# Kernel tuning notes

Measured on AMD Instinct MI355X. Metric: run time of the kernel, lower is better.

The kernel has to match this reference:

```python
import jax, jax.numpy as jnp
import numpy as np

B, NB, S, K, M, C = 2, 6000, 3, 8, 6, 256
INIT = 0.02


def setup_inputs() -> dict:
    key = jax.random.key(0)
    ks = jax.random.split(key, 24)
    d = {}
    d["pts_query_feats"] = jax.random.normal(ks[0], (B, NB, C), jnp.float32)
    d["pts_query_pe"] = jax.random.normal(ks[1], (B, NB, C), jnp.float32)
    d["knn_feat_seq"] = jax.random.normal(ks[2], (S, B, NB, K, C), jnp.float32)
    d["knn_pe_seq"] = jax.random.normal(ks[3], (S, B, NB, K, C), jnp.float32)
    d["sampled_feat"] = jax.random.normal(ks[4], (B, NB, M, C), jnp.float32)
    d["mask"] = jax.random.bernoulli(ks[5], 0.7, (B, NB, M))  # True = valid image sample
    # per-seq temporal attention params (S cloned single-head MHA modules)
    d["Wq_t"] = INIT * jax.random.normal(ks[6], (S, C, C), jnp.float32)
    d["Wk_t"] = INIT * jax.random.normal(ks[7], (S, C, C), jnp.float32)
    d["Wv_t"] = INIT * jax.random.normal(ks[8], (S, C, C), jnp.float32)
    d["Wo_t"] = INIT * jax.random.normal(ks[9], (S, C, C), jnp.float32)
    d["bq_t"] = jnp.zeros((S, C), jnp.float32)
    d["bk_t"] = jnp.zeros((S, C), jnp.float32)
    d["bv_t"] = jnp.zeros((S, C), jnp.float32)
    d["bo_t"] = jnp.zeros((S, C), jnp.float32)
    # cross-sensor single-head MHA params
    d["Wq_c"] = INIT * jax.random.normal(ks[10], (C, C), jnp.float32)
    d["Wk_c"] = INIT * jax.random.normal(ks[11], (C, C), jnp.float32)
    d["Wv_c"] = INIT * jax.random.normal(ks[12], (C, C), jnp.float32)
    d["Wo_c"] = INIT * jax.random.normal(ks[13], (C, C), jnp.float32)
    d["bq_c"] = jnp.zeros((C,), jnp.float32)
    d["bk_c"] = jnp.zeros((C,), jnp.float32)
    d["bv_c"] = jnp.zeros((C,), jnp.float32)
    d["bo_c"] = jnp.zeros((C,), jnp.float32)
    return d


def reference(pts_query_feats, pts_query_pe, knn_feat_seq, knn_pe_seq,
              sampled_feat, mask,
              Wq_t, Wk_t, Wv_t, Wo_t, bq_t, bk_t, bv_t, bo_t,
              Wq_c, Wk_c, Wv_c, Wo_c, bq_c, bk_c, bv_c, bo_c):
    scale = 1.0 / np.sqrt(C).astype(np.float32)

    # with_pos_embed
    q_base = pts_query_feats + pts_query_pe           # [B,NB,C]
    kv = knn_feat_seq + knn_pe_seq                    # [S,B,NB,K,C]

    # temporal attention: per voxel, 1 query token attends over K knn keys;
    # S distinct (cloned) single-head MHA modules, outputs summed over seq.
    q = jnp.einsum('bnc,scd->sbnd', q_base, Wq_t) + bq_t[:, None, None, :]
    k = jnp.einsum('sbnkc,scd->sbnkd', kv, Wk_t) + bk_t[:, None, None, None, :]
    v = jnp.einsum('sbnkc,scd->sbnkd', kv, Wv_t) + bv_t[:, None, None, None, :]
    scores = jnp.einsum('sbnd,sbnkd->sbnk', q, k) * scale
    attn = jax.nn.softmax(scores, axis=-1)
    ctx = jnp.einsum('sbnk,sbnkd->sbnd', attn, v)
    out_s = jnp.einsum('sbnd,sde->sbne', ctx, Wo_t) + bo_t[:, None, None, :]
    out = out_s.sum(axis=0)                           # [B,NB,C]

    # cross-sensor attention over M image samples; attn_mask = ~mask (True blocks)
    valid = mask.any(axis=-1)                         # [B,NB]
    qc = out @ Wq_c + bq_c                            # [B,NB,C]
    kc = sampled_feat @ Wk_c + bk_c                   # [B,NB,M,C]
    vc = sampled_feat @ Wv_c + bv_c
    sc = jnp.einsum('bnc,bnmc->bnm', qc, kc) * scale
    sc = jnp.where(mask, sc, -1e9)
    a = jax.nn.softmax(sc, axis=-1)
    cctx = jnp.einsum('bnm,bnmc->bnc', a, vc)
    outc = cctx @ Wo_c + bo_c                         # [B,NB,C]

    # original drops invalid voxels; we keep static shape and zero them
    return jnp.where(valid[..., None], outc, 0.0)
```

## Files before the change

### kernel.cpp

```cpp
#include <hip/hip_runtime.h>
#include <math.h>

#define CC 256
#define KK 8
#define MM 6
#define SS 3
#define NVOX 12000
#define VB 16
#define NBLK (NVOX / VB)

typedef __attribute__((ext_vector_type(8))) short bf16x8;
typedef __attribute__((ext_vector_type(4))) float f32x4;
typedef __attribute__((ext_vector_type(4))) float fvec4;

#define OFF_WQKF3  0u
#define OFF_WVOF   262144u
#define OFF_BQK    1048576u
#define OFF_BVO    1052672u
#define OFF_BBIG   1056768u
#define OFF_QK3PK  1057792u
#define OFF_WBIGPK 1451008u
#define OFF_WVOCPK 1844224u
#define WS_NEED    1975296u

__device__ __forceinline__ float wred(float p) {
  #pragma unroll
  for (int off = 32; off; off >>= 1) p += __shfl_xor(p, off, 64);
  return p;
}
__device__ __forceinline__ uint f2bf(float x) {
  const uint u = __float_as_uint(x);
  return (u + 0x7fffu + ((u >> 16) & 1u)) >> 16;
}
__device__ __forceinline__ uint bfpack(float a, float b) {
  return (f2bf(b) << 16) | f2bf(a);
}
__device__ __forceinline__ float bflo(uint w) { return __uint_as_float(w << 16); }
__device__ __forceinline__ float bfhi(uint w) { return __uint_as_float(w & 0xffff0000u); }

__device__ __forceinline__ f32x4 mfma16(bf16x8 a, bf16x8 b, f32x4 c) {
  return __builtin_amdgcn_mfma_f32_16x16x32_bf16(a, b, c, 0, 0, 0);
}

__global__ __launch_bounds__(256) void prep_fold_all(
    const float* __restrict__ Wq_t, const float* __restrict__ Wq_c,
    const float* __restrict__ Wk_t, const float* __restrict__ Wk_c,
    const float* __restrict__ Wv_t, const float* __restrict__ Wv_c,
    const float* __restrict__ Wo_t, const float* __restrict__ Wo_c,
    const float* __restrict__ bq_t, const float* __restrict__ bq_c,
    const float* __restrict__ bv_t, const float* __restrict__ bv_c,
    const float* __restrict__ bo_t, const float* __restrict__ bo_c,
    float* __restrict__ Wqkf3, float* __restrict__ Wvof,
    float* __restrict__ bqk, float* __restrict__ bvo,
    uint4* __restrict__ qk3pk, uint4* __restrict__ wvocpk) {
  const int b = blockIdx.x, t = threadIdx.x;
  if (b < 256) {
    const int u = b >> 5, c0 = (b & 31) * 8;
    __shared__ float xl[8][256];
    const float* X;
    if (u < 4) X = (u < 3) ? (Wq_t + u * 65536) : Wq_c;
    else { const int v = u - 4; X = (v < 3) ? (Wv_t + v * 65536) : Wv_c; }
    #pragma unroll
    for (int i = 0; i < 8; ++i) xl[i][t] = X[(c0 + i) * 256 + t];
    __syncthreads();
    float acc[8] = {0.f, 0.f, 0.f, 0.f, 0.f, 0.f, 0.f, 0.f};
    if (u < 4) {
      const float* Wk = (u < 3) ? (Wk_t + u * 65536) : Wk_c;
      const float4* wr = (const float4*)(Wk + t * 256);
      #pragma unroll 4
      for (int d4 = 0; d4 < 64; ++d4) {
        const float4 wv = wr[d4];
        #pragma unroll
        for (int j = 0; j < 8; ++j) {
          acc[j] += xl[j][d4 * 4] * wv.x + xl[j][d4 * 4 + 1] * wv.y +
                    xl[j][d4 * 4 + 2] * wv.z + xl[j][d4 * 4 + 3] * wv.w;
        }
      }
    } else {
      const int v = u - 4;
      const float* Wo = (v < 3) ? (Wo_t + v * 65536) : Wo_c;
      #pragma unroll 4
      for (int d = 0; d < 256; ++d) {
        const float w = Wo[d * 256 + t];
        #pragma unroll
        for (int j = 0; j < 8; ++j) acc[j] += xl[j][d] * w;
      }
    }
    const int lane = (((c0 >> 3) & 3) << 4) | (t & 15);
    if (u < 3) {
      uint4 o;
      o.x = bfpack(acc[0], acc[1]); o.y = bfpack(acc[2], acc[3]);
      o.z = bfpack(acc[4], acc[5]); o.w = bfpack(acc[6], acc[7]);
      qk3pk[((u * 16 + (t >> 4)) * 8 + (c0 >> 5)) * 64 + lane] = o;
    } else if (u == 3) {
      #pragma unroll
      for (int j = 0; j < 8; ++j) Wqkf3[(c0 + j) * 256 + t] = acc[j];
    } else if (u < 7) {
      const int v = u - 4;
      #pragma unroll
      for (int j = 0; j < 8; ++j) Wvof[(v * 256 + c0 + j) * 256 + t] = acc[j];
    } else {
      uint4 o;
      o.x = bfpack(acc[0], acc[1]); o.y = bfpack(acc[2], acc[3]);
      o.z = bfpack(acc[4], acc[5]); o.w = bfpack(acc[6], acc[7]);
      wvocpk[((t >> 4) * 8 + (c0 >> 5)) * 64 + lane] = o;
    }
  } else {
    const int u = b - 256;
    __shared__ float bql[256], bvl[256];
    const float* bq = (u < 3) ? (bq_t + u * 256) : bq_c;
    const float* bv = (u < 3) ? (bv_t + u * 256) : bv_c;
    const float* bo = (u < 3) ? (bo_t + u * 256) : bo_c;
    bql[t] = bq[t]; bvl[t] = bv[t];
    __syncthreads();
    const float* Wk = (u < 3) ? (Wk_t + u * 65536) : Wk_c;
    const float* Wo = (u < 3) ? (Wo_t + u * 65536) : Wo_c;
    const float4* wr = (const float4*)(Wk + t * 256);
    float a1 = 0.f, a2 = 0.f;
    #pragma unroll 4
    for (int d4 = 0; d4 < 64; ++d4) {
      const float4 wv = wr[d4];
      a1 += bql[d4 * 4] * wv.x + bql[d4 * 4 + 1] * wv.y +
            bql[d4 * 4 + 2] * wv.z + bql[d4 * 4 + 3] * wv.w;
    }
    #pragma unroll 4
    for (int d = 0; d < 256; ++d) a2 += bvl[d] * Wo[d * 256 + t];
    bqk[u * 256 + t] = a1;
    bvo[u * 256 + t] = a2 + bo[t];
  }
}

__global__ __launch_bounds__(256) void prep_wbig2(
    const float* __restrict__ Wvof, const float* __restrict__ Wqkf3,
    const float* __restrict__ bqk, const float* __restrict__ bvo,
    uint4* __restrict__ wbigpk, float* __restrict__ bbig) {
  const int b = blockIdx.x, t = threadIdx.x;
  if (b < 96) {
    const int c0 = b * 8;
    __shared__ float xl[8][256];
    #pragma unroll
    for (int i = 0; i < 8; ++i) xl[i][t] = Wvof[(c0 + i) * 256 + t];
    __syncthreads();
    float acc[8] = {0.f, 0.f, 0.f, 0.f, 0.f, 0.f, 0.f, 0.f};
    #pragma unroll 4
    for (int d = 0; d < 256; ++d) {
      const float w = Wqkf3[d * 256 + t];
      #pragma unroll
      for (int j = 0; j < 8; ++j) acc[j] += xl[j][d] * w;
    }
    uint4 o;
    o.x = bfpack(acc[0], acc[1]); o.y = bfpack(acc[2], acc[3]);
    o.z = bfpack(acc[4], acc[5]); o.w = bfpack(acc[6], acc[7]);
    const int lane = (((c0 >> 3) & 3) << 4) | (t & 15);
    wbigpk[((t >> 4) * 24 + (c0 >> 5)) * 64 + lane] = o;
  } else {
    __shared__ float bvs[256];
    bvs[t] = bvo[t] + bvo[256 + t] + bvo[512 + t];
    __syncthreads();
    float acc = bqk[3 * 256 + t];
    #pragma unroll 4
    for (int d = 0; d < 256; ++d) acc += bvs[d] * Wqkf3[d * 256 + t];
    bbig[t] = acc;
  }
}

__global__ __launch_bounds__(512, 4) void stftr_mega(
    const float* __restrict__ ptsf, const float* __restrict__ ptspe,
    const float* __restrict__ knnf, const float* __restrict__ knnpe,
    const float* __restrict__ sfeat, const int* __restrict__ maskp,
    const bf16x8* __restrict__ qk3pk, const bf16x8* __restrict__ wbigpk,
    const bf16x8* __restrict__ wvocpk,
    const float* __restrict__ bqk, const float* __restrict__ bbig,
    const float* __restrict__ bvoc,
    float* __restrict__ out) {
  __shared__ char shA[25088];
  __shared__ char shB[24832];
  __shared__ int vlds[VB];
  const int t = threadIdx.x, lane = t & 63, w = t >> 6;
  const int g0 = blockIdx.x * VB;

  {
    uint* qb_u = (uint*)shB;
    const float4* a4 = (const float4*)(ptsf + (size_t)g0 * CC);
    const float4* b4 = (const float4*)(ptspe + (size_t)g0 * CC);
    #pragma unroll
    for (int it = 0; it < 2; ++it) {
      const int idx = it * 512 + t;
      const int row = idx >> 6, c4 = idx & 63;
      const float4 va = a4[idx], vb = b4[idx];
      qb_u[row * 132 + c4 * 2]     = bfpack(va.x + vb.x, va.y + vb.y);
      qb_u[row * 132 + c4 * 2 + 1] = bfpack(va.z + vb.z, va.w + vb.w);
    }
  }
  __syncthreads();
  {
    f32x4 acc[6];
    #pragma unroll
    for (int nb = 0; nb < 6; ++nb) acc[nb] = (f32x4){0.f, 0.f, 0.f, 0.f};
    const char* qbase = shB + (lane & 15) * 528 + (lane >> 4) * 16;
    #pragma unroll
    for (int kb = 0; kb < 8; ++kb) {
      const bf16x8 a = *(const bf16x8*)(qbase + kb * 64);
      #pragma unroll
      for (int nb = 0; nb < 6; ++nb) {
        const bf16x8 bb = qk3pk[((w * 6 + nb) * 8 + kb) * 64 + lane];
        acc[nb] = mfma16(a, bb, acc[nb]);
      }
    }
    ushort* us = (ushort*)shA;
    #pragma unroll
    for (int nb = 0; nb < 6; ++nb) {
      const int n = (w * 6 + nb) * 16 + (lane & 15);
      const float bias = bqk[n];
      #pragma unroll
      for (int r = 0; r < 4; ++r) {
        const int row = (lane >> 4) * 4 + r;
        us[row * 776 + n] = (ushort)f2bf(acc[nb][r] + bias);
      }
    }
  }
  __syncthreads();
  {
    const uint* Au = (const uint*)shA;
    uint* Bu = (uint*)shB;
    const fvec4* kfp = (const fvec4*)knnf;
    const fvec4* kpp = (const fvec4*)knnpe;
    #pragma unroll
    for (int q = 0; q < 6; ++q) {
      const int tid = w * 6 + q;
      const int s = tid >> 4, j = tid & 15;
      const size_t rb = ((size_t)(s * NVOX + g0 + j)) * 512 + lane;
      fvec4 sm[KK];
      #pragma unroll
      for (int r = 0; r < KK; ++r) {
        const fvec4 kf = __builtin_nontemporal_load(&kfp[rb + r * 64]);
        const fvec4 kp = __builtin_nontemporal_load(&kpp[rb + r * 64]);
        sm[r] = kf + kp;
      }
      const uint ua = Au[j * 388 + s * 128 + lane * 2];
      const uint ub = Au[j * 388 + s * 128 + lane * 2 + 1];
      const float u0 = bflo(ua), u1 = bfhi(ua), u2 = bflo(ub), u3 = bfhi(ub);
      float sc[KK];
      #pragma unroll
      for (int r = 0; r < KK; ++r) {
        float p = sm[r].x * u0 + sm[r].y * u1 + sm[r].z * u2 + sm[r].w * u3;
        sc[r] = wred(p);
      }
      float mx = sc[0];
      #pragma unroll
      for (int r = 1; r < KK; ++r) mx = fmaxf(mx, sc[r]);
      float e[KK], sum = 0.f;
      #pragma unroll
      for (int r = 0; r < KK; ++r) { e[r] = __expf((sc[r] - mx) * 0.0625f); sum += e[r]; }
      const float inv = 1.f / sum;
      fvec4 acc = (fvec4){0.f, 0.f, 0.f, 0.f};
      #pragma unroll
      for (int r = 0; r < KK; ++r) acc += (e[r] * inv) * sm[r];
      Bu[j * 388 + s * 128 + lane * 2]     = bfpack(acc.x, acc.y);
      Bu[j * 388 + s * 128 + lane * 2 + 1] = bfpack(acc.z, acc.w);
    }
  }
  __syncthreads();
  {
    f32x4 acc[2];
    acc[0] = (f32x4){0.f, 0.f, 0.f, 0.f};
    acc[1] = (f32x4){0.f, 0.f, 0.f, 0.f};
    const char* abase = shB + (lane & 15) * 1552 + (lane >> 4) * 16;
    #pragma unroll 4
    for (int kb = 0; kb < 24; ++kb) {
      const bf16x8 a = *(const bf16x8*)(abase + kb * 64);
      #pragma unroll
      for (int nb = 0; nb < 2; ++nb) {
        const bf16x8 bb = wbigpk[((w * 2 + nb) * 24 + kb) * 64 + lane];
        acc[nb] = mfma16(a, bb, acc[nb]);
      }
    }
    ushort* ust = (ushort*)shA;
    #pragma unroll
    for (int nb = 0; nb < 2; ++nb) {
      const int n = (w * 2 + nb) * 16 + (lane & 15);
      const float bias = bbig[n];
      #pragma unroll
      for (int r = 0; r < 4; ++r) {
        const int row = (lane >> 4) * 4 + r;
        ust[row * 264 + n] = (ushort)f2bf(acc[nb][r] + bias);
      }
    }
  }
  __syncthreads();
  {
    const uint* Au = (const uint*)shA;
    uint* Bu = (uint*)shB;
    const float4* sfp = (const float4*)sfeat;
    #pragma unroll
    for (int jj = 0; jj < 2; ++jj) {
      const int j = w * 2 + jj;
      const int g = g0 + j;
      const uint ua = Au[j * 132 + lane * 2];
      const uint ub = Au[j * 132 + lane * 2 + 1];
      const float u0 = bflo(ua), u1 = bfhi(ua), u2 = bflo(ub), u3 = bfhi(ub);
      const size_t sb = (size_t)g * (MM * 64) + lane;
      float4 sf[MM]; float scm[MM]; int anyv = 0;
      #pragma unroll
      for (int m = 0; m < MM; ++m) {
        sf[m] = sfp[sb + m * 64];
        const int mk = maskp[(size_t)g * MM + m];
        anyv |= mk;
        float p = sf[m].x * u0 + sf[m].y * u1 + sf[m].z * u2 + sf[m].w * u3;
        p = wred(p);
        scm[m] = mk ? p * 0.0625f : -1e9f;
      }
      float mx = scm[0];
      #pragma unroll
      for (int m = 1; m < MM; ++m) mx = fmaxf(mx, scm[m]);
      float e[MM], sum = 0.f;
      #pragma unroll
      for (int m = 0; m < MM; ++m) { e[m] = __expf(scm[m] - mx); sum += e[m]; }
      const float inv = 1.f / sum;
      float4 ag = make_float4(0.f, 0.f, 0.f, 0.f);
      #pragma unroll
      for (int m = 0; m < MM; ++m) {
        const float a = e[m] * inv;
        ag.x += a * sf[m].x; ag.y += a * sf[m].y;
        ag.z += a * sf[m].z; ag.w += a * sf[m].w;
      }
      Bu[j * 132 + lane * 2]     = bfpack(ag.x, ag.y);
      Bu[j * 132 + lane * 2 + 1] = bfpack(ag.z, ag.w);
      if (lane == 0) vlds[j] = anyv;
    }
  }
  __syncthreads();
  {
    f32x4 acc[2];
    acc[0] = (f32x4){0.f, 0.f, 0.f, 0.f};
    acc[1] = (f32x4){0.f, 0.f, 0.f, 0.f};
    const char* cbase = shB + (lane & 15) * 528 + (lane >> 4) * 16;
    #pragma unroll
    for (int kb = 0; kb < 8; ++kb) {
      const bf16x8 a = *(const bf16x8*)(cbase + kb * 64);
      #pragma unroll
      for (int nb = 0; nb < 2; ++nb) {
        const bf16x8 bb = wvocpk[((w * 2 + nb) * 8 + kb) * 64 + lane];
        acc[nb] = mfma16(a, bb, acc[nb]);
      }
    }
    float* ost = (float*)(shA + 8448);
    #pragma unroll
    for (int nb = 0; nb < 2; ++nb) {
      const int n = (w * 2 + nb) * 16 + (lane & 15);
      const float bias = bvoc[n];
      #pragma unroll
      for (int r = 0; r < 4; ++r) {
        const int row = (lane >> 4) * 4 + r;
        ost[row * 260 + n] = acc[nb][r] + bias;
      }
    }
  }
  __syncthreads();
  {
    const float* ost = (const float*)(shA + 8448);
    #pragma unroll
    for (int it = 0; it < 8; ++it) {
      const int idx = it * 512 + t;
      const int row = idx >> 8, d = idx & 255;
      out[((size_t)(g0 + row)) * 256 + d] = vlds[row] ? ost[row * 260 + d] : 0.f;
    }
  }
}

extern "C" void kernel_launch(void* const* d_in, const int* in_sizes, int n_in,
                              void* d_out, int out_size, void* d_ws, size_t ws_size,
                              hipStream_t stream) {
  const float* ptsf  = (const float*)d_in[0];
  const float* ptspe = (const float*)d_in[1];
  const float* knnf  = (const float*)d_in[2];
  const float* knnpe = (const float*)d_in[3];
  const float* sfeat = (const float*)d_in[4];
  const int*   maskp = (const int*)d_in[5];
  const float* Wq_t = (const float*)d_in[6];
  const float* Wk_t = (const float*)d_in[7];
  const float* Wv_t = (const float*)d_in[8];
  const float* Wo_t = (const float*)d_in[9];
  const float* bq_t = (const float*)d_in[10];
  const float* bv_t = (const float*)d_in[12];
  const float* bo_t = (const float*)d_in[13];
  const float* Wq_c = (const float*)d_in[14];
  const float* Wk_c = (const float*)d_in[15];
  const float* Wv_c = (const float*)d_in[16];
  const float* Wo_c = (const float*)d_in[17];
  const float* bq_c = (const float*)d_in[18];
  const float* bv_c = (const float*)d_in[20];
  const float* bo_c = (const float*)d_in[21];

  if (ws_size < WS_NEED) return;
  char* ws = (char*)d_ws;
  float* Wqkf3  = (float*)(ws + OFF_WQKF3);
  float* Wvof   = (float*)(ws + OFF_WVOF);
  float* bqk    = (float*)(ws + OFF_BQK);
  float* bvo    = (float*)(ws + OFF_BVO);
  float* bbig   = (float*)(ws + OFF_BBIG);
  uint4* qk3pk  = (uint4*)(ws + OFF_QK3PK);
  uint4* wbigpk = (uint4*)(ws + OFF_WBIGPK);
  uint4* wvocpk = (uint4*)(ws + OFF_WVOCPK);

  prep_fold_all<<<260, 256, 0, stream>>>(
      Wq_t, Wq_c, Wk_t, Wk_c, Wv_t, Wv_c, Wo_t, Wo_c,
      bq_t, bq_c, bv_t, bv_c, bo_t, bo_c,
      Wqkf3, Wvof, bqk, bvo, qk3pk, wvocpk);
  prep_wbig2<<<97, 256, 0, stream>>>(Wvof, Wqkf3, bqk, bvo, wbigpk, bbig);

  stftr_mega<<<NBLK, 512, 0, stream>>>(
      ptsf, ptspe, knnf, knnpe, sfeat, maskp,
      (const bf16x8*)qk3pk, (const bf16x8*)wbigpk, (const bf16x8*)wvocpk,
      bqk, bbig, bvo + 3 * 256, (float*)d_out);
}
```

Measured before the change: 171.2 us.

## Merge weight-fold prep kernels into one and tune main kernel memory access

Merges the two weight-folding prep kernels into a single launch. Each block now chains the Wv·Wo·Wq_c·Wk_c products itself, which removes the intermediate fp32 workspace and the dependency between two launches. The main kernel raises its occupancy hint from 4 to 6 waves per SIMD and stages the mask in LDS instead of reading it per lane. It also uses nontemporal loads and stores for streamed inputs and output, and drops an unroll on the KNN loop. Tradeoffs: the prep blocks do serial work, and the higher occupancy target may cause register spills.

Measured after the change: 170.2 us. About the same (-0.6%).

```diff
diff --git a/kernel.cpp b/kernel.cpp
--- a/kernel.cpp
+++ b/kernel.cpp
@@ -13,15 +13,13 @@
 typedef __attribute__((ext_vector_type(4))) float f32x4;
 typedef __attribute__((ext_vector_type(4))) float fvec4;
 
-#define OFF_WQKF3  0u
-#define OFF_WVOF   262144u
-#define OFF_BQK    1048576u
-#define OFF_BVO    1052672u
-#define OFF_BBIG   1056768u
-#define OFF_QK3PK  1057792u
-#define OFF_WBIGPK 1451008u
-#define OFF_WVOCPK 1844224u
-#define WS_NEED    1975296u
+#define OFF_QK3PK  0u
+#define OFF_WBIGPK 393216u
+#define OFF_WVOCPK 786432u
+#define OFF_BQK    917504u
+#define OFF_BBIG   920576u
+#define OFF_BVOC   921600u
+#define WS_NEED    922624u
 
 __device__ __forceinline__ float wred(float p) {
   #pragma unroll
@@ -42,7 +40,7 @@
   return __builtin_amdgcn_mfma_f32_16x16x32_bf16(a, b, c, 0, 0, 0);
 }
 
-__global__ __launch_bounds__(256) void prep_fold_all(
+__global__ __launch_bounds__(256) void prep_all(
     const float* __restrict__ Wq_t, const float* __restrict__ Wq_c,
     const float* __restrict__ Wk_t, const float* __restrict__ Wk_c,
     const float* __restrict__ Wv_t, const float* __restrict__ Wv_c,
@@ -50,121 +48,145 @@
     const float* __restrict__ bq_t, const float* __restrict__ bq_c,
     const float* __restrict__ bv_t, const float* __restrict__ bv_c,
     const float* __restrict__ bo_t, const float* __restrict__ bo_c,
-    float* __restrict__ Wqkf3, float* __restrict__ Wvof,
-    float* __restrict__ bqk, float* __restrict__ bvo,
-    uint4* __restrict__ qk3pk, uint4* __restrict__ wvocpk) {
+    uint4* __restrict__ qk3pk, uint4* __restrict__ wbigpk,
+    uint4* __restrict__ wvocpk,
+    float* __restrict__ bqk, float* __restrict__ bbig,
+    float* __restrict__ bvoc) {
   const int b = blockIdx.x, t = threadIdx.x;
-  if (b < 256) {
+  __shared__ float xl[8][256];
+  if (b < 96) {
     const int u = b >> 5, c0 = (b & 31) * 8;
-    __shared__ float xl[8][256];
-    const float* X;
-    if (u < 4) X = (u < 3) ? (Wq_t + u * 65536) : Wq_c;
-    else { const int v = u - 4; X = (v < 3) ? (Wv_t + v * 65536) : Wv_c; }
-    #pragma unroll
-    for (int i = 0; i < 8; ++i) xl[i][t] = X[(c0 + i) * 256 + t];
+    const float* Wq = Wq_t + u * 65536;
+    const float* Wk = Wk_t + u * 65536;
+    #pragma unroll
+    for (int i = 0; i < 8; ++i) xl[i][t] = Wq[(c0 + i) * 256 + t];
     __syncthreads();
     float acc[8] = {0.f, 0.f, 0.f, 0.f, 0.f, 0.f, 0.f, 0.f};
-    if (u < 4) {
-      const float* Wk = (u < 3) ? (Wk_t + u * 65536) : Wk_c;
-      const float4* wr = (const float4*)(Wk + t * 256);
-      #pragma unroll 4
-      for (int d4 = 0; d4 < 64; ++d4) {
-        const float4 wv = wr[d4];
-        #pragma unroll
-        for (int j = 0; j < 8; ++j) {
-          acc[j] += xl[j][d4 * 4] * wv.x + xl[j][d4 * 4 + 1] * wv.y +
-                    xl[j][d4 * 4 + 2] * wv.z + xl[j][d4 * 4 + 3] * wv.w;
-        }
-      }
-    } else {
-      const int v = u - 4;
-      const float* Wo = (v < 3) ? (Wo_t + v * 65536) : Wo_c;
-      #pragma unroll 4
-      for (int d = 0; d < 256; ++d) {
-        const float w = Wo[d * 256 + t];
-        #pragma unroll
-        for (int j = 0; j < 8; ++j) acc[j] += xl[j][d] * w;
-      }
-    }
-    const int lane = (((c0 >> 3) & 3) << 4) | (t & 15);
-    if (u < 3) {
-      uint4 o;
-      o.x = bfpack(acc[0], acc[1]); o.y = bfpack(acc[2], acc[3]);
-      o.z = bfpack(acc[4], acc[5]); o.w = bfpack(acc[6], acc[7]);
-      qk3pk[((u * 16 + (t >> 4)) * 8 + (c0 >> 5)) * 64 + lane] = o;
-    } else if (u == 3) {
-      #pragma unroll
-      for (int j = 0; j < 8; ++j) Wqkf3[(c0 + j) * 256 + t] = acc[j];
-    } else if (u < 7) {
-      const int v = u - 4;
-      #pragma unroll
-      for (int j = 0; j < 8; ++j) Wvof[(v * 256 + c0 + j) * 256 + t] = acc[j];
-    } else {
-      uint4 o;
-      o.x = bfpack(acc[0], acc[1]); o.y = bfpack(acc[2], acc[3]);
-      o.z = bfpack(acc[4], acc[5]); o.w = bfpack(acc[6], acc[7]);
-      wvocpk[((t >> 4) * 8 + (c0 >> 5)) * 64 + lane] = o;
-    }
-  } else {
-    const int u = b - 256;
-    __shared__ float bql[256], bvl[256];
-    const float* bq = (u < 3) ? (bq_t + u * 256) : bq_c;
-    const float* bv = (u < 3) ? (bv_t + u * 256) : bv_c;
-    const float* bo = (u < 3) ? (bo_t + u * 256) : bo_c;
-    bql[t] = bq[t]; bvl[t] = bv[t];
-    __syncthreads();
-    const float* Wk = (u < 3) ? (Wk_t + u * 65536) : Wk_c;
-    const float* Wo = (u < 3) ? (Wo_t + u * 65536) : Wo_c;
     const float4* wr = (const float4*)(Wk + t * 256);
-    float a1 = 0.f, a2 = 0.f;
     #pragma unroll 4
     for (int d4 = 0; d4 < 64; ++d4) {
       const float4 wv = wr[d4];
-      a1 += bql[d4 * 4] * wv.x + bql[d4 * 4 + 1] * wv.y +
-            bql[d4 * 4 + 2] * wv.z + bql[d4 * 4 + 3] * wv.w;
-    }
-    #pragma unroll 4
-    for (int d = 0; d < 256; ++d) a2 += bvl[d] * Wo[d * 256 + t];
-    bqk[u * 256 + t] = a1;
-    bvo[u * 256 + t] = a2 + bo[t];
-  }
-}
-
-__global__ __launch_bounds__(256) void prep_wbig2(
-    const float* __restrict__ Wvof, const float* __restrict__ Wqkf3,
-    const float* __restrict__ bqk, const float* __restrict__ bvo,
-    uint4* __restrict__ wbigpk, float* __restrict__ bbig) {
-  const int b = blockIdx.x, t = threadIdx.x;
-  if (b < 96) {
-    const int c0 = b * 8;
-    __shared__ float xl[8][256];
-    #pragma unroll
-    for (int i = 0; i < 8; ++i) xl[i][t] = Wvof[(c0 + i) * 256 + t];
-    __syncthreads();
-    float acc[8] = {0.f, 0.f, 0.f, 0.f, 0.f, 0.f, 0.f, 0.f};
-    #pragma unroll 4
-    for (int d = 0; d < 256; ++d) {
-      const float w = Wqkf3[d * 256 + t];
-      #pragma unroll
-      for (int j = 0; j < 8; ++j) acc[j] += xl[j][d] * w;
-    }
+      #pragma unroll
+      for (int j = 0; j < 8; ++j)
+        acc[j] += xl[j][d4 * 4] * wv.x + xl[j][d4 * 4 + 1] * wv.y +
+                  xl[j][d4 * 4 + 2] * wv.z + xl[j][d4 * 4 + 3] * wv.w;
+    }
+    const int lane = (((c0 >> 3) & 3) << 4) | (t & 15);
     uint4 o;
     o.x = bfpack(acc[0], acc[1]); o.y = bfpack(acc[2], acc[3]);
     o.z = bfpack(acc[4], acc[5]); o.w = bfpack(acc[6], acc[7]);
+    qk3pk[((u * 16 + (t >> 4)) * 8 + (c0 >> 5)) * 64 + lane] = o;
+  } else if (b < 192) {
+    const int v = (b - 96) >> 5, bi = (b - 96) & 31;
+    const int c0 = bi * 8, row0 = v * 256 + c0;
+    const float* Wv = Wv_t + v * 65536;
+    const float* Wo = Wo_t + v * 65536;
+    #pragma unroll
+    for (int i = 0; i < 8; ++i) xl[i][t] = Wv[(c0 + i) * 256 + t];
+    __syncthreads();
+    float a1[8] = {0.f, 0.f, 0.f, 0.f, 0.f, 0.f, 0.f, 0.f};
+    #pragma unroll 4
+    for (int d = 0; d < 256; ++d) {
+      const float w = Wo[d * 256 + t];
+      #pragma unroll
+      for (int j = 0; j < 8; ++j) a1[j] += xl[j][d] * w;
+    }
+    __syncthreads();
+    #pragma unroll
+    for (int j = 0; j < 8; ++j) xl[j][t] = a1[j];
+    __syncthreads();
+    float a2[8] = {0.f, 0.f, 0.f, 0.f, 0.f, 0.f, 0.f, 0.f};
+    #pragma unroll 4
+    for (int d = 0; d < 256; ++d) {
+      const float w = Wq_c[d * 256 + t];
+      #pragma unroll
+      for (int j = 0; j < 8; ++j) a2[j] += xl[j][d] * w;
+    }
+    __syncthreads();
+    #pragma unroll
+    for (int j = 0; j < 8; ++j) xl[j][t] = a2[j];
+    __syncthreads();
+    float a3[8] = {0.f, 0.f, 0.f, 0.f, 0.f, 0.f, 0.f, 0.f};
+    const float4* wr = (const float4*)(Wk_c + t * 256);
+    #pragma unroll 4
+    for (int d4 = 0; d4 < 64; ++d4) {
+      const float4 wv = wr[d4];
+      #pragma unroll
+      for (int j = 0; j < 8; ++j)
+        a3[j] += xl[j][d4 * 4] * wv.x + xl[j][d4 * 4 + 1] * wv.y +
+                 xl[j][d4 * 4 + 2] * wv.z + xl[j][d4 * 4 + 3] * wv.w;
+    }
+    const int lane = (((row0 >> 3) & 3) << 4) | (t & 15);
+    uint4 o;
+    o.x = bfpack(a3[0], a3[1]); o.y = bfpack(a3[2], a3[3]);
+    o.z = bfpack(a3[4], a3[5]); o.w = bfpack(a3[6], a3[7]);
+    wbigpk[((t >> 4) * 24 + (row0 >> 5)) * 64 + lane] = o;
+  } else if (b < 224) {
+    const int c0 = (b - 192) * 8;
+    #pragma unroll
+    for (int i = 0; i < 8; ++i) xl[i][t] = Wv_c[(c0 + i) * 256 + t];
+    __syncthreads();
+    float acc[8] = {0.f, 0.f, 0.f, 0.f, 0.f, 0.f, 0.f, 0.f};
+    #pragma unroll 4
+    for (int d = 0; d < 256; ++d) {
+      const float w = Wo_c[d * 256 + t];
+      #pragma unroll
+      for (int j = 0; j < 8; ++j) acc[j] += xl[j][d] * w;
+    }
     const int lane = (((c0 >> 3) & 3) << 4) | (t & 15);
-    wbigpk[((t >> 4) * 24 + (c0 >> 5)) * 64 + lane] = o;
+    uint4 o;
+    o.x = bfpack(acc[0], acc[1]); o.y = bfpack(acc[2], acc[3]);
+    o.z = bfpack(acc[4], acc[5]); o.w = bfpack(acc[6], acc[7]);
+    wvocpk[((t >> 4) * 8 + (c0 >> 5)) * 64 + lane] = o;
+  } else if (b < 227) {
+    const int u = b - 224;
+    xl[0][t] = bq_t[u * 256 + t];
+    __syncthreads();
+    const float4* wr = (const float4*)(Wk_t + u * 65536 + t * 256);
+    float a = 0.f;
+    #pragma unroll 4
+    for (int d4 = 0; d4 < 64; ++d4) {
+      const float4 wv = wr[d4];
+      a += xl[0][d4 * 4] * wv.x + xl[0][d4 * 4 + 1] * wv.y +
+           xl[0][d4 * 4 + 2] * wv.z + xl[0][d4 * 4 + 3] * wv.w;
+    }
+    bqk[u * 256 + t] = a;
   } else {
-    __shared__ float bvs[256];
-    bvs[t] = bvo[t] + bvo[256 + t] + bvo[512 + t];
-    __syncthreads();
-    float acc = bqk[3 * 256 + t];
-    #pragma unroll 4
-    for (int d = 0; d < 256; ++d) acc += bvs[d] * Wqkf3[d * 256 + t];
-    bbig[t] = acc;
-  }
-}
-
-__global__ __launch_bounds__(512, 4) void stftr_mega(
+    xl[0][t] = bv_t[t]; xl[1][t] = bv_t[256 + t];
+    xl[2][t] = bv_t[512 + t]; xl[3][t] = bv_c[t];
+    __syncthreads();
+    float bvs = bo_t[t] + bo_t[256 + t] + bo_t[512 + t];
+    float bvc = bo_c[t];
+    #pragma unroll 2
+    for (int d = 0; d < 256; ++d) {
+      bvs += xl[0][d] * Wo_t[d * 256 + t] +
+             xl[1][d] * Wo_t[65536 + d * 256 + t] +
+             xl[2][d] * Wo_t[131072 + d * 256 + t];
+      bvc += xl[3][d] * Wo_c[d * 256 + t];
+    }
+    bvoc[t] = bvc;
+    __syncthreads();
+    xl[4][t] = bvs;
+    __syncthreads();
+    float y = bq_c[t];
+    #pragma unroll 4
+    for (int d = 0; d < 256; ++d) y += xl[4][d] * Wq_c[d * 256 + t];
+    __syncthreads();
+    xl[5][t] = y;
+    __syncthreads();
+    const float4* wr = (const float4*)(Wk_c + t * 256);
+    float bb = 0.f;
+    #pragma unroll 4
+    for (int d4 = 0; d4 < 64; ++d4) {
+      const float4 wv = wr[d4];
+      bb += xl[5][d4 * 4] * wv.x + xl[5][d4 * 4 + 1] * wv.y +
+            xl[5][d4 * 4 + 2] * wv.z + xl[5][d4 * 4 + 3] * wv.w;
+    }
+    bbig[t] = bb;
+  }
+}
+
+__global__ __launch_bounds__(512, 6) void stftr_mega(
     const float* __restrict__ ptsf, const float* __restrict__ ptspe,
     const float* __restrict__ knnf, const float* __restrict__ knnpe,
     const float* __restrict__ sfeat, const int* __restrict__ maskp,
@@ -175,22 +197,25 @@
     float* __restrict__ out) {
   __shared__ char shA[25088];
   __shared__ char shB[24832];
+  __shared__ int mlds[VB * MM];
   __shared__ int vlds[VB];
   const int t = threadIdx.x, lane = t & 63, w = t >> 6;
   const int g0 = blockIdx.x * VB;
 
   {
     uint* qb_u = (uint*)shB;
-    const float4* a4 = (const float4*)(ptsf + (size_t)g0 * CC);
-    const float4* b4 = (const float4*)(ptspe + (size_t)g0 * CC);
+    const fvec4* a4 = (const fvec4*)(ptsf + (size_t)g0 * CC);
+    const fvec4* b4 = (const fvec4*)(ptspe + (size_t)g0 * CC);
     #pragma unroll
     for (int it = 0; it < 2; ++it) {
       const int idx = it * 512 + t;
       const int row = idx >> 6, c4 = idx & 63;
-      const float4 va = a4[idx], vb = b4[idx];
+      const fvec4 va = __builtin_nontemporal_load(&a4[idx]);
+      const fvec4 vb = __builtin_nontemporal_load(&b4[idx]);
       qb_u[row * 132 + c4 * 2]     = bfpack(va.x + vb.x, va.y + vb.y);
       qb_u[row * 132 + c4 * 2 + 1] = bfpack(va.z + vb.z, va.w + vb.w);
     }
+    if (t < VB * MM) mlds[t] = maskp[g0 * MM + t];
   }
   __syncthreads();
   {
@@ -225,7 +250,6 @@
     uint* Bu = (uint*)shB;
     const fvec4* kfp = (const fvec4*)knnf;
     const fvec4* kpp = (const fvec4*)knnpe;
-    #pragma unroll
     for (int q = 0; q < 6; ++q) {
       const int tid = w * 6 + q;
       const int s = tid >> 4, j = tid & 15;
@@ -291,7 +315,7 @@
   {
     const uint* Au = (const uint*)shA;
     uint* Bu = (uint*)shB;
-    const float4* sfp = (const float4*)sfeat;
+    const fvec4* sfp = (const fvec4*)sfeat;
     #pragma unroll
     for (int jj = 0; jj < 2; ++jj) {
       const int j = w * 2 + jj;
@@ -300,11 +324,11 @@
       const uint ub = Au[j * 132 + lane * 2 + 1];
       const float u0 = bflo(ua), u1 = bfhi(ua), u2 = bflo(ub), u3 = bfhi(ub);
       const size_t sb = (size_t)g * (MM * 64) + lane;
-      float4 sf[MM]; float scm[MM]; int anyv = 0;
+      fvec4 sf[MM]; float scm[MM]; int anyv = 0;
       #pragma unroll
       for (int m = 0; m < MM; ++m) {
-        sf[m] = sfp[sb + m * 64];
-        const int mk = maskp[(size_t)g * MM + m];
+        sf[m] = __builtin_nontemporal_load(&sfp[sb + m * 64]);
+        const int mk = mlds[j * MM + m];
         anyv |= mk;
         float p = sf[m].x * u0 + sf[m].y * u1 + sf[m].z * u2 + sf[m].w * u3;
         p = wred(p);
@@ -317,13 +341,9 @@
       #pragma unroll
       for (int m = 0; m < MM; ++m) { e[m] = __expf(scm[m] - mx); sum += e[m]; }
       const float inv = 1.f / sum;
-      float4 ag = make_float4(0.f, 0.f, 0.f, 0.f);
-      #pragma unroll
-      for (int m = 0; m < MM; ++m) {
-        const float a = e[m] * inv;
-        ag.x += a * sf[m].x; ag.y += a * sf[m].y;
-        ag.z += a * sf[m].z; ag.w += a * sf[m].w;
-      }
+      fvec4 ag = (fvec4){0.f, 0.f, 0.f, 0.f};
+      #pragma unroll
+      for (int m = 0; m < MM; ++m) ag += (e[m] * inv) * sf[m];
       Bu[j * 132 + lane * 2]     = bfpack(ag.x, ag.y);
       Bu[j * 132 + lane * 2 + 1] = bfpack(ag.z, ag.w);
       if (lane == 0) vlds[j] = anyv;
@@ -363,7 +383,8 @@
     for (int it = 0; it < 8; ++it) {
       const int idx = it * 512 + t;
       const int row = idx >> 8, d = idx & 255;
-      out[((size_t)(g0 + row)) * 256 + d] = vlds[row] ? ost[row * 260 + d] : 0.f;
+      const float v = vlds[row] ? ost[row * 260 + d] : 0.f;
+      __builtin_nontemporal_store(v, &out[((size_t)(g0 + row)) * 256 + d]);
     }
   }
 }
@@ -394,23 +415,20 @@
 
   if (ws_size < WS_NEED) return;
   char* ws = (char*)d_ws;
-  float* Wqkf3  = (float*)(ws + OFF_WQKF3);
-  float* Wvof   = (float*)(ws + OFF_WVOF);
-  float* bqk    = (float*)(ws + OFF_BQK);
-  float* bvo    = (float*)(ws + OFF_BVO);
-  float* bbig   = (float*)(ws + OFF_BBIG);
   uint4* qk3pk  = (uint4*)(ws + OFF_QK3PK);
   uint4* wbigpk = (uint4*)(ws + OFF_WBIGPK);
   uint4* wvocpk = (uint4*)(ws + OFF_WVOCPK);
-
-  prep_fold_all<<<260, 256, 0, stream>>>(
+  float* bqk    = (float*)(ws + OFF_BQK);
+  float* bbig   = (float*)(ws + OFF_BBIG);
+  float* bvoc   = (float*)(ws + OFF_BVOC);
+
+  prep_all<<<228, 256, 0, stream>>>(
       Wq_t, Wq_c, Wk_t, Wk_c, Wv_t, Wv_c, Wo_t, Wo_c,
       bq_t, bq_c, bv_t, bv_c, bo_t, bo_c,
-      Wqkf3, Wvof, bqk, bvo, qk3pk, wvocpk);
-  prep_wbig2<<<97, 256, 0, stream>>>(Wvof, Wqkf3, bqk, bvo, wbigpk, bbig);
+      qk3pk, wbigpk, wvocpk, bqk, bbig, bvoc);
 
   stftr_mega<<<NBLK, 512, 0, stream>>>(
       ptsf, ptspe, knnf, knnpe, sfeat, maskp,
       (const bf16x8*)qk3pk, (const bf16x8*)wbigpk, (const bf16x8*)wvocpk,
-      bqk, bbig, bvo + 3 * 256, (float*)d_out);
-}
+      bqk, bbig, bvoc, (float*)d_out);
+}
```
